# Performance work log

Measured on AMD Instinct MI355X. Metric: run time of the kernel, lower is better.

The kernel has to match this reference:

```python
import jax, jax.numpy as jnp
import numpy as np

EPS = 1e-10            # safe_log epsilon
SIGMOID_BETA = 1.0
MLE_STEP_SIZE = 0.01
NUM_MLE_STEPS = 15
ENT_MULT = 0.01        # entropy loss multiplier placeholder
DECAY_MULT = 0.001     # weight decay multiplier placeholder
B, P, N, T = 512, 1024, 1024, 32


def sigmoid(a, beta=SIGMOID_BETA):
    # module's rescaled sigmoid: 2/(1+exp(-beta*a)) - 1, range (-1, 1)
    return 2.0 / (1.0 + jnp.exp(-beta * a)) - 1.0


def tri_basis(a_sig, centers):
    # triangle basis functions: relu(1 - |a - c_j| / width), width = center spacing
    # a_sig [B,N], centers [T] -> [B,N,T]
    width = centers[1] - centers[0]
    return jax.nn.relu(1.0 - jnp.abs(a_sig[..., None] - centers) / width)


def prob_est(a_sig, thetas, centers):
    # per-neuron mixture of triangle kernels; mixture weights = softmax(thetas)
    pi = jax.nn.softmax(thetas, axis=1)               # [N,T]
    return jnp.einsum('bnt,nt->bn', tri_basis(a_sig, centers), pi)  # [B,N]


def log_likelihood(a_sig, thetas, centers):
    return jnp.sum(jnp.log(prob_est(a_sig, thetas, centers) + EPS))


def calc_entropy(probs):
    # per-neuron entropy reduction over the batch axis
    return -jnp.sum(probs * jnp.log(probs + EPS), axis=0)  # [N]


def setup_inputs() -> dict:
    key = jax.random.key(0)
    k0, k1, k2, k3 = jax.random.split(key, 4)
    x = jax.random.normal(k0, (B, P), jnp.float32)
    w_enc = 0.5 * jax.random.normal(k1, (P, N), jnp.float32)   # truncated_normal std 0.5 approx
    b_enc = 0.1 * jax.random.normal(k2, (N,), jnp.float32)
    w_dec = jnp.transpose(w_enc)                                # initialized as w_enc^T
    b_dec = 0.1 * jax.random.normal(k3, (P,), jnp.float32)
    thetas = jnp.ones((N, T), jnp.float32)                      # construct_thetas init
    triangle_centers = jnp.linspace(-1.0, 1.0, T).astype(jnp.float32)  # a_sig range
    return {"x": x, "w_enc": w_enc, "b_enc": b_enc, "w_dec": w_dec,
            "b_dec": b_dec, "thetas": thetas, "triangle_centers": triangle_centers}


def reference(x, w_enc, b_enc, w_dec, b_dec, thetas, triangle_centers):
    # --- inference: relu encoder (noise_var_mult = 0 -> deterministic a) ---
    a = jax.nn.relu(x @ w_enc + b_enc)                # [B,N]
    a_sig = sigmoid(a, SIGMOID_BETA)                  # [B,N] in (-1,1)

    # --- iterative MLE gradient-ascent on thetas (num_mle_steps updates) ---
    ll_grad = jax.grad(lambda th: log_likelihood(a_sig, th, triangle_centers))

    def mle_step(th, _):
        return th + MLE_STEP_SIZE * ll_grad(th), None

    thetas_new, _ = jax.lax.scan(mle_step, thetas, None, length=NUM_MLE_STEPS)

    # --- entropy of the triangle-kernel density estimate ---
    probs = prob_est(a_sig, thetas_new, triangle_centers)   # [B,N]
    a_entropies = calc_entropy(probs)                       # [N]

    # --- decoder / losses ---
    x_hat = a @ w_dec + b_dec                               # [B,P]
    recon_loss = jnp.mean(0.5 * jnp.sum((x - x_hat) ** 2, axis=1))
    entropy_loss = ENT_MULT * jnp.sum(a_entropies)
    # tf.nn.l2_loss(t) = sum(t^2)/2
    decay_loss = 0.5 * DECAY_MULT * (0.5 * jnp.sum(w_enc ** 2) + 0.5 * jnp.sum(w_dec ** 2))
    total_loss = recon_loss + entropy_loss + decay_loss
    return x_hat, a_entropies, total_loss
```

## Files before the change

kernel.cpp:

```cpp
#include <hip/hip_runtime.h>

#define EPSC 1e-10f
#define BDIM 512
#define PDIM 1024
#define NDIM 1024
#define TDIM 32

typedef __attribute__((ext_vector_type(8))) short short8;
typedef __attribute__((ext_vector_type(4))) float f32x4;

static __device__ __forceinline__ short f2bf(float f) {
  unsigned u = __float_as_uint(f);
  unsigned r = (u + 0x7fffu + ((u >> 16) & 1u)) >> 16;
  return (short)r;
}

__global__ __launch_bounds__(256) void conv_kernel(
    const float* __restrict__ X, const float* __restrict__ W1, const float* __restrict__ W2,
    short* __restrict__ Xsw, short* __restrict__ T1, short* __restrict__ T2,
    float* __restrict__ pwsq)
{
  int tid = threadIdx.x;
  if (blockIdx.x < 256) {
    int i = blockIdx.x * 256 + tid;
    int m = i >> 7, c = i & 127;
    const float* src = X + (size_t)m * 1024 + c * 8;
    float4 v0 = *(const float4*)src;
    float4 v1 = *(const float4*)(src + 4);
    short8 o;
    o[0] = f2bf(v0.x); o[1] = f2bf(v0.y); o[2] = f2bf(v0.z); o[3] = f2bf(v0.w);
    o[4] = f2bf(v1.x); o[5] = f2bf(v1.y); o[6] = f2bf(v1.z); o[7] = f2bf(v1.w);
    *(short8*)(Xsw + ((size_t)((m >> 4) * 32 + (c >> 2)) * 512) + (c & 3) * 128 + (m & 15) * 8) = o;
    return;
  }
  __shared__ float T[64][65];
  __shared__ float red[4];
  int wb = blockIdx.x - 256;
  int z = wb >> 8;
  int w = wb & 255;
  int r0 = (w >> 4) * 64;
  int c0 = (w & 15) * 64;
  const float* src = z ? W2 : W1;
  short* dst = z ? T2 : T1;
  float wsq = 0.0f;
#pragma unroll
  for (int i = 0; i < 4; ++i) {
    int row = (tid >> 4) + i * 16;
    int col = (tid & 15) << 2;
    float4 v = *(const float4*)(src + (size_t)(r0 + row) * NDIM + c0 + col);
    T[row][col + 0] = v.x; T[row][col + 1] = v.y; T[row][col + 2] = v.z; T[row][col + 3] = v.w;
    wsq = fmaf(v.x, v.x, wsq); wsq = fmaf(v.y, v.y, wsq);
    wsq = fmaf(v.z, v.z, wsq); wsq = fmaf(v.w, v.w, wsq);
  }
  __syncthreads();
  int nl = tid >> 2;
  int kb = (tid & 3) << 4;
  int ng = c0 + nl;
  int nt = ng >> 4, rn = ng & 15;
#pragma unroll
  for (int h = 0; h < 2; ++h) {
    int kg = r0 + kb + 8 * h;
    int kc = kg >> 5, q = (kg >> 3) & 3;
    short8 o;
#pragma unroll
    for (int e = 0; e < 8; ++e) o[e] = f2bf(T[kb + 8 * h + e][nl]);
    *(short8*)(dst + ((size_t)(nt * 32 + kc) * 512) + q * 128 + rn * 8) = o;
  }
#pragma unroll
  for (int d = 32; d >= 1; d >>= 1) wsq += __shfl_xor(wsq, d);
  if ((tid & 63) == 0) red[tid >> 6] = wsq;
  __syncthreads();
  if (tid == 0) pwsq[wb] = red[0] + red[1] + red[2] + red[3];
}

__global__ __launch_bounds__(256) void gemm1_mfma(
    const short* __restrict__ Xsw, const short* __restrict__ Wsw,
    const float* __restrict__ bias, const float* __restrict__ centers,
    short* __restrict__ Absw, float* __restrict__ U, int* __restrict__ ticket)
{
  __shared__ float T2s[32][36];
  int tid = threadIdx.x;
  if (blockIdx.x == 0 && blockIdx.y == 0 && tid == 0) *ticket = 0;
  int lane = tid & 63, wid = tid >> 6;
  int wy = wid >> 1, wx = wid & 1;
  int mt = blockIdx.y * 2 + wy;
  int nt = blockIdx.x * 2 + wx;
  const short* ap = Xsw + (size_t)mt * 16384 + lane * 8;
  const short* bp = Wsw + (size_t)nt * 16384 + lane * 8;
  f32x4 acc = {0.f, 0.f, 0.f, 0.f};
#pragma unroll 8
  for (int kc = 0; kc < 32; ++kc) {
    short8 a = *(const short8*)(ap + kc * 512);
    short8 b = *(const short8*)(bp + kc * 512);
    acc = __builtin_amdgcn_mfma_f32_16x16x32_bf16(a, b, acc, 0, 0, 0);
  }
  int q = lane >> 4, r = lane & 15;
  int nn = nt * 16 + r;
  float bi = bias[nn];
  float c0 = centers[0];
  float invw = 1.0f / (centers[1] - centers[0]);
  short* abase = Absw + ((size_t)(mt * 32 + (nn >> 5)) * 512) + ((nn >> 3) & 3) * 128 + (nn & 7);
#pragma unroll
  for (int rr = 0; rr < 4; ++rr) {
    int rm = q * 4 + rr;
    float a = fmaxf(acc[rr] + bi, 0.0f);
    abase[rm * 8] = f2bf(a);
    T2s[wx * 16 + r][wy * 16 + rm] = (2.0f / (1.0f + __expf(-a)) - 1.0f - c0) * invw;
  }
  __syncthreads();
  int row = tid >> 3;
  int col4 = (tid & 7) << 2;
  float4 uv = make_float4(T2s[row][col4], T2s[row][col4 + 1], T2s[row][col4 + 2], T2s[row][col4 + 3]);
  *(float4*)(U + (size_t)(blockIdx.x * 32 + row) * BDIM + blockIdx.y * 32 + col4) = uv;
}

__global__ __launch_bounds__(256) void gemm2_mfma(
    const short* __restrict__ Absw, const short* __restrict__ Wdsw,
    const float* __restrict__ bias, const float* __restrict__ X,
    float* __restrict__ out, float* __restrict__ precon)
{
  __shared__ float red[4];
  int tid = threadIdx.x;
  int lane = tid & 63, wid = tid >> 6;
  int wy = wid >> 1, wx = wid & 1;
  int mt = blockIdx.y * 2 + wy;
  int nt = blockIdx.x * 2 + wx;
  const short* ap = Absw + (size_t)mt * 16384 + lane * 8;
  const short* bp = Wdsw + (size_t)nt * 16384 + lane * 8;
  f32x4 acc = {0.f, 0.f, 0.f, 0.f};
#pragma unroll 8
  for (int kc = 0; kc < 32; ++kc) {
    short8 a = *(const short8*)(ap + kc * 512);
    short8 b = *(const short8*)(bp + kc * 512);
    acc = __builtin_amdgcn_mfma_f32_16x16x32_bf16(a, b, acc, 0, 0, 0);
  }
  int q = lane >> 4, r = lane & 15;
  int nn = nt * 16 + r;
  float bi = bias[nn];
  float local = 0.0f;
#pragma unroll
  for (int rr = 0; rr < 4; ++rr) {
    int mm = mt * 16 + q * 4 + rr;
    float xh = acc[rr] + bi;
    out[(size_t)mm * PDIM + nn] = xh;
    float d = xh - X[(size_t)mm * PDIM + nn];
    local = fmaf(d, d, local);
  }
#pragma unroll
  for (int d = 32; d >= 1; d >>= 1) local += __shfl_xor(local, d);
  if ((tid & 63) == 0) red[tid >> 6] = local;
  __syncthreads();
  if (tid == 0) precon[blockIdx.y * 32 + blockIdx.x] = red[0] + red[1] + red[2] + red[3];
}

__global__ __launch_bounds__(64) void mle_kernel(
    const float* __restrict__ U, const float* __restrict__ thetas,
    float* __restrict__ ent_out, const float* __restrict__ precon,
    const float* __restrict__ pwsq, int* __restrict__ ticket, float* __restrict__ out)
{
  int n = blockIdx.x;
  int lane = threadIdx.x;
  __shared__ float s_s[128 * 34];
  __shared__ int tick_s;

  float f_reg[8];
  int j_reg[8];
#pragma unroll
  for (int i = 0; i < 8; i++) {
    float u = U[(size_t)n * BDIM + lane + i * 64];
    int j = (int)u;
    if (j > TDIM - 2) j = TDIM - 2;
    if (j < 0) j = 0;
    f_reg[i] = u - (float)j;
    j_reg[i] = j;
  }
  float th = (lane < TDIM) ? thetas[(size_t)n * TDIM + lane] : 0.0f;

  int base0 = lane * 34;
  int base1 = (lane + 64) * 34;
  int h = lane >> 5, t = lane & 31;
  float pv = 0.0f;

  for (int step = 0; step < 15; ++step) {
    float tv = __shfl(th, lane & 31);
    float mx = tv;
#pragma unroll
    for (int d = 16; d >= 1; d >>= 1) mx = fmaxf(mx, __shfl_xor(mx, d));
    float e = __expf(tv - mx);
    float se = e;
#pragma unroll
    for (int d = 16; d >= 1; d >>= 1) se += __shfl_xor(se, d);
    pv = e / se;
#pragma unroll
    for (int i = 0; i < 17; i++) {
      *(float2*)&s_s[base0 + 2 * i] = make_float2(0.f, 0.f);
      *(float2*)&s_s[base1 + 2 * i] = make_float2(0.f, 0.f);
    }
    float S_local = 0.0f;
#pragma unroll
    for (int i = 0; i < 8; i++) {
      int j = j_reg[i];
      float f = f_reg[i];
      float pj  = __shfl(pv, j);
      float pj1 = __shfl(pv, j + 1);
      float p = (1.0f - f) * pj + f * pj1;
      float r = 1.0f / (p + EPSC);
      S_local = fmaf(p, r, S_local);
      float* sp = &s_s[(i < 4 ? base0 : base1) + j];
      sp[0] += (1.0f - f) * r;
      sp[1] += f * r;
    }
    __syncthreads();
    float S = S_local;
#pragma unroll
    for (int d = 32; d >= 1; d >>= 1) S += __shfl_xor(S, d);
    float colsum = 0.0f;
#pragma unroll 8
    for (int L = 0; L < 64; ++L) colsum += s_s[(h * 64 + L) * 34 + t];
    colsum += __shfl_xor(colsum, 32);
    if (lane < TDIM) th += 0.01f * pv * (colsum - S);
    __syncthreads();
  }

  float tv = __shfl(th, lane & 31);
  float mx = tv;
#pragma unroll
  for (int d = 16; d >= 1; d >>= 1) mx = fmaxf(mx, __shfl_xor(mx, d));
  float e = __expf(tv - mx);
  float se = e;
#pragma unroll
  for (int d = 16; d >= 1; d >>= 1) se += __shfl_xor(se, d);
  pv = e / se;
  float ent_local = 0.0f;
#pragma unroll
  for (int i = 0; i < 8; i++) {
    int j = j_reg[i];
    float f = f_reg[i];
    float p = (1.0f - f) * __shfl(pv, j) + f * __shfl(pv, j + 1);
    ent_local = fmaf(p, __logf(p + EPSC), ent_local);
  }
  float E = ent_local;
#pragma unroll
  for (int d = 32; d >= 1; d >>= 1) E += __shfl_xor(E, d);
  if (lane == 0) ent_out[n] = -E;

  __threadfence();
  if (lane == 0) tick_s = atomicAdd(ticket, 1);
  __syncthreads();
  if (tick_s == NDIM - 1) {
    __threadfence();
    const volatile float* ev = (const volatile float*)ent_out;
    float acc = 0.0f;
#pragma unroll
    for (int i = 0; i < 16; i++) acc += 0.01f * ev[lane + i * 64];
#pragma unroll
    for (int i = 0; i < 8; i++) acc += (0.5f / (float)BDIM) * precon[lane + i * 64];
#pragma unroll
    for (int i = 0; i < 8; i++) acc += 0.00025f * pwsq[lane + i * 64];
#pragma unroll
    for (int d = 32; d >= 1; d >>= 1) acc += __shfl_xor(acc, d);
    if (lane == 0) out[(size_t)BDIM * PDIM + NDIM] = acc;
  }
}

extern "C" void kernel_launch(void* const* d_in, const int* in_sizes, int n_in,
                              void* d_out, int out_size, void* d_ws, size_t ws_size,
                              hipStream_t stream) {
  (void)in_sizes; (void)n_in; (void)out_size; (void)ws_size;
  const float* x       = (const float*)d_in[0];
  const float* w_enc   = (const float*)d_in[1];
  const float* b_enc   = (const float*)d_in[2];
  const float* w_dec   = (const float*)d_in[3];
  const float* b_dec   = (const float*)d_in[4];
  const float* thetas  = (const float*)d_in[5];
  const float* centers = (const float*)d_in[6];
  float* out = (float*)d_out;

  char* ws = (char*)d_ws;
  short* Xsw    = (short*)(ws);
  short* Wsw    = (short*)(ws + (1 << 20));
  short* Wdsw   = (short*)(ws + (3 << 20));
  short* Absw   = (short*)(ws + (5 << 20));
  float* U      = (float*)(ws + (6 << 20));
  float* precon = (float*)(ws + (8 << 20));
  float* pwsq   = (float*)(ws + (8 << 20) + 4096);
  int*   ticket = (int*)(ws + (8 << 20) + 8192);
  float* ent_out = out + (size_t)BDIM * PDIM;

  hipLaunchKernelGGL(conv_kernel, dim3(768), dim3(256), 0, stream,
                     x, w_enc, w_dec, Xsw, Wsw, Wdsw, pwsq);
  hipLaunchKernelGGL(gemm1_mfma, dim3(32, 16), dim3(256), 0, stream,
                     Xsw, Wsw, b_enc, centers, Absw, U, ticket);
  hipLaunchKernelGGL(gemm2_mfma, dim3(32, 16), dim3(256), 0, stream,
                     Absw, Wdsw, b_dec, x, out, precon);
  hipLaunchKernelGGL(mle_kernel, dim3(NDIM), dim3(64), 0, stream,
                     U, thetas, ent_out, precon, pwsq, ticket, out);
}
```

Before: 159.0 us.

## Use non-negative activation range to shrink MLE histogram into per-lane registers

Because the encoder output is post-ReLU, the sigmoid is non-negative and only the upper 17 triangle bins can be hit. The MLE kernel now keeps per-lane 17-bin histograms in registers and does a single LDS transpose-reduce per step, instead of zeroing and scattering into a 128x34 shared array with barriers. It also drops the softmax max-subtraction, replaces the computed sum of p/(p+eps) with the constant 512, and uses a fast reciprocal and vectorized loads of U. The cost removed is shared-memory traffic, barriers and reduction work per step. In exchange, correctness now depends on thetas staying small enough for exp not to overflow and on eps being negligible.

```diff
diff --git a/kernel.cpp b/kernel.cpp
--- a/kernel.cpp
+++ b/kernel.cpp
@@ -160,89 +160,83 @@
 {
   int n = blockIdx.x;
   int lane = threadIdx.x;
-  __shared__ float s_s[128 * 34];
+  __shared__ float s_s[64 * 17];
   __shared__ int tick_s;
 
-  float f_reg[8];
-  int j_reg[8];
-#pragma unroll
-  for (int i = 0; i < 8; i++) {
-    float u = U[(size_t)n * BDIM + lane + i * 64];
-    int j = (int)u;
-    if (j > TDIM - 2) j = TDIM - 2;
-    if (j < 0) j = 0;
-    f_reg[i] = u - (float)j;
-    j_reg[i] = j;
-  }
-  float th = (lane < TDIM) ? thetas[(size_t)n * TDIM + lane] : 0.0f;
-
-  int base0 = lane * 34;
-  int base1 = (lane + 64) * 34;
-  int h = lane >> 5, t = lane & 31;
+  const float4* up = (const float4*)(U + (size_t)n * BDIM + lane * 8);
+  float4 u0 = up[0], u1 = up[1];
+  float uu[8] = {u0.x, u0.y, u0.z, u0.w, u1.x, u1.y, u1.z, u1.w};
+  float f[8]; int jl[8];
+#pragma unroll
+  for (int i = 0; i < 8; ++i) {
+    int j = (int)uu[i];
+    if (j > 30) j = 30;
+    if (j < 15) j = 15;
+    f[i] = uu[i] - (float)j;
+    jl[i] = j - 15;
+  }
+  float th = thetas[(size_t)n * TDIM + (lane & 31)];
+  int t2 = lane & 31;
+  int rb = t2 < 17 ? t2 : 16;
+  int csbase = (lane >> 5) * 32;
   float pv = 0.0f;
 
+#pragma unroll 1
   for (int step = 0; step < 15; ++step) {
-    float tv = __shfl(th, lane & 31);
-    float mx = tv;
-#pragma unroll
-    for (int d = 16; d >= 1; d >>= 1) mx = fmaxf(mx, __shfl_xor(mx, d));
-    float e = __expf(tv - mx);
+    float e = __expf(th);
     float se = e;
 #pragma unroll
     for (int d = 16; d >= 1; d >>= 1) se += __shfl_xor(se, d);
     pv = e / se;
-#pragma unroll
-    for (int i = 0; i < 17; i++) {
-      *(float2*)&s_s[base0 + 2 * i] = make_float2(0.f, 0.f);
-      *(float2*)&s_s[base1 + 2 * i] = make_float2(0.f, 0.f);
+
+    float bins[17];
+#pragma unroll
+    for (int t = 0; t < 17; ++t) bins[t] = 0.0f;
+#pragma unroll
+    for (int i = 0; i < 8; ++i) {
+      float pj  = __shfl(pv, jl[i] + 15);
+      float pj1 = __shfl(pv, jl[i] + 16);
+      float p = fmaf(f[i], pj1 - pj, pj);
+      float r = __builtin_amdgcn_rcpf(p + EPSC);
+      float w0 = (1.0f - f[i]) * r;
+      float w1 = f[i] * r;
+#pragma unroll
+      for (int t = 0; t < 17; ++t)
+        bins[t] += (jl[i] == t) ? w0 : ((jl[i] + 1 == t) ? w1 : 0.0f);
     }
-    float S_local = 0.0f;
-#pragma unroll
-    for (int i = 0; i < 8; i++) {
-      int j = j_reg[i];
-      float f = f_reg[i];
-      float pj  = __shfl(pv, j);
-      float pj1 = __shfl(pv, j + 1);
-      float p = (1.0f - f) * pj + f * pj1;
-      float r = 1.0f / (p + EPSC);
-      S_local = fmaf(p, r, S_local);
-      float* sp = &s_s[(i < 4 ? base0 : base1) + j];
-      sp[0] += (1.0f - f) * r;
-      sp[1] += f * r;
-    }
-    __syncthreads();
-    float S = S_local;
-#pragma unroll
-    for (int d = 32; d >= 1; d >>= 1) S += __shfl_xor(S, d);
-    float colsum = 0.0f;
+
+#pragma unroll
+    for (int t = 0; t < 17; ++t) s_s[lane * 17 + t] = bins[t];
+
+    float part = 0.0f;
 #pragma unroll 8
-    for (int L = 0; L < 64; ++L) colsum += s_s[(h * 64 + L) * 34 + t];
-    colsum += __shfl_xor(colsum, 32);
-    if (lane < TDIM) th += 0.01f * pv * (colsum - S);
-    __syncthreads();
-  }
-
-  float tv = __shfl(th, lane & 31);
-  float mx = tv;
-#pragma unroll
-  for (int d = 16; d >= 1; d >>= 1) mx = fmaxf(mx, __shfl_xor(mx, d));
-  float e = __expf(tv - mx);
-  float se = e;
-#pragma unroll
-  for (int d = 16; d >= 1; d >>= 1) se += __shfl_xor(se, d);
-  pv = e / se;
-  float ent_local = 0.0f;
-#pragma unroll
-  for (int i = 0; i < 8; i++) {
-    int j = j_reg[i];
-    float f = f_reg[i];
-    float p = (1.0f - f) * __shfl(pv, j) + f * __shfl(pv, j + 1);
-    ent_local = fmaf(p, __logf(p + EPSC), ent_local);
-  }
-  float E = ent_local;
-#pragma unroll
-  for (int d = 32; d >= 1; d >>= 1) E += __shfl_xor(E, d);
-  if (lane == 0) ent_out[n] = -E;
+    for (int L = 0; L < 32; ++L) part += s_s[(csbase + L) * 17 + rb];
+    part += __shfl(part, (lane & 31) + 32);
+
+    int src = t2 - 15;
+    float sv = __shfl(part, src < 0 ? 0 : src);
+    if (src < 0) sv = 0.0f;
+    th += 0.01f * pv * (sv - 512.0f);
+  }
+
+  {
+    float e = __expf(th);
+    float se = e;
+#pragma unroll
+    for (int d = 16; d >= 1; d >>= 1) se += __shfl_xor(se, d);
+    pv = e / se;
+  }
+  float ent = 0.0f;
+#pragma unroll
+  for (int i = 0; i < 8; ++i) {
+    float pj  = __shfl(pv, jl[i] + 15);
+    float pj1 = __shfl(pv, jl[i] + 16);
+    float p = fmaf(f[i], pj1 - pj, pj);
+    ent = fmaf(p, __logf(p + EPSC), ent);
+  }
+#pragma unroll
+  for (int d = 32; d >= 1; d >>= 1) ent += __shfl_xor(ent, d);
+  if (lane == 0) ent_out[n] = -ent;
 
   __threadfence();
   if (lane == 0) tick_s = atomicAdd(ticket, 1);
```

Result: slower. 171.2 us (+7.7%).
